# Kernel optimization log

Measured on AMD Instinct MI355X. Metric: run time of the kernel, lower is better.

The kernel has to match this reference:

```python
import jax, jax.numpy as jnp
import numpy as np

EPS = 1e-12


def _segment_softmax(logits, seg, n):
    # numerically stable softmax over edges grouped by destination node
    m = jax.ops.segment_max(logits, seg, num_segments=n)
    e = jnp.exp(logits - m[seg])
    s = jax.ops.segment_sum(e, seg, num_segments=n)
    return e / s[seg]


def _agnn(x, src, dst, beta, n):
    # cosine-similarity attention (PyG AGNNConv): alpha_ij = softmax_i(beta * <x_i/|x_i|, x_j/|x_j|>)
    norm = jnp.sqrt(jnp.sum(x * x, axis=-1, keepdims=True))
    xn = x / jnp.maximum(norm, EPS)
    logits = beta * jnp.sum(xn[dst] * xn[src], axis=-1)  # [E+N]
    alpha = _segment_softmax(logits, dst, n)
    return jax.ops.segment_sum(alpha[:, None] * x[src], dst, num_segments=n)


def setup_inputs() -> dict:
    key = jax.random.key(0)
    ks = jax.random.split(key, 6)
    N, E, F, H, C = 100000, 3200000, 512, 16, 7
    x = jax.random.normal(ks[0], (N, F), dtype=jnp.float32)
    edge_index = jax.random.randint(ks[1], (2, E), 0, N, dtype=jnp.int32)
    W1 = jax.random.normal(ks[2], (H, F), dtype=jnp.float32) * 0.05
    b1 = jnp.zeros((H,), jnp.float32)
    W2 = jax.random.normal(ks[3], (C, H), dtype=jnp.float32) * 0.2
    b2 = jnp.zeros((C,), jnp.float32)
    return {
        "x": x, "edge_index": edge_index,
        "W1": W1, "b1": b1,
        "beta2": jnp.ones((1,), jnp.float32),
        "beta3": jnp.ones((1,), jnp.float32),
        "beta4": jnp.ones((1,), jnp.float32),
        "W2": W2, "b2": b2,
    }


def reference(x, edge_index, W1, b1, beta2, beta3, beta4, W2, b2):
    N = x.shape[0]
    loop = jnp.arange(N, dtype=edge_index.dtype)
    src = jnp.concatenate([edge_index[0], loop])  # self-loops added by AGNNConv
    dst = jnp.concatenate([edge_index[1], loop])

    h = jax.nn.relu(x @ W1.T + b1)                 # lin1 on raw features (eval: dropout = id)
    h = _agnn(h, src, dst, jnp.float32(1.0), N)    # prop1: beta fixed at 1 (requires_grad=False)
    h = _agnn(h, src, dst, beta2[0], N)
    h = _agnn(h, src, dst, beta3[0], N)
    h = _agnn(h, src, dst, beta4[0], N)
    logits = h @ W2.T + b2
    return jax.nn.log_softmax(logits, axis=1)
```

## Files before the change

kernel.cpp:

```cpp
#include <hip/hip_runtime.h>
#include <hip/hip_fp16.h>
#include <math.h>

#define F 512
#define H 16
#define C 7
#define NB 512
#define BIN_CHUNK 4096
#define BIN_T 512

typedef _Float16 h2 __attribute__((ext_vector_type(2)));

__device__ __forceinline__ h2 as_h2(unsigned u) { return __builtin_bit_cast(h2, u); }
__device__ __forceinline__ unsigned as_u32(h2 v) { return __builtin_bit_cast(unsigned, v); }

__device__ __forceinline__ float dot2acc(h2 a, h2 b, float c) {
#if __has_builtin(__builtin_amdgcn_fdot2)
    return __builtin_amdgcn_fdot2(a, b, c, false);
#else
    return c + (float)a[0] * (float)b[0] + (float)a[1] * (float)b[1];
#endif
}

__device__ __forceinline__ float rsq(float x) {
#if __has_builtin(__builtin_amdgcn_rsqf)
    return __builtin_amdgcn_rsqf(x);
#else
    return rsqrtf(x);
#endif
}

__global__ void zero_i32(int* p, int n) {
    int i = blockIdx.x * blockDim.x + threadIdx.x;
    if (i < n) p[i] = 0;
}

__global__ __launch_bounds__(BIN_T) void bin_edges(const int* __restrict__ ei, int E, int Etot,
                                                   int width, int cap, int* __restrict__ gcnt,
                                                   unsigned* __restrict__ binned) {
    __shared__ int cnt[NB];
    __shared__ int base[NB];
    int t = threadIdx.x;
    for (int i = t; i < NB; i += BIN_T) cnt[i] = 0;
    __syncthreads();
    long chunk0 = (long)blockIdx.x * BIN_CHUNK;
    for (int k = 0; k < BIN_CHUNK / BIN_T; ++k) {
        long e = chunk0 + k * BIN_T + t;
        if (e < Etot) {
            int dst = (e < E) ? ei[E + e] : (int)(e - E);
            atomicAdd(&cnt[dst / width], 1);
        }
    }
    __syncthreads();
    for (int i = t; i < NB; i += BIN_T) {
        int c = cnt[i];
        base[i] = c ? atomicAdd(&gcnt[i], c) : 0;
        cnt[i] = 0;
    }
    __syncthreads();
    for (int k = 0; k < BIN_CHUNK / BIN_T; ++k) {
        long e = chunk0 + k * BIN_T + t;
        if (e < Etot) {
            int src, dst;
            if (e < E) { src = ei[e]; dst = ei[E + e]; }
            else       { src = (int)(e - E); dst = src; }
            int b = dst / width;
            size_t pos = (size_t)b * cap + base[b] + atomicAdd(&cnt[b], 1);
            binned[pos] = (unsigned)src | ((unsigned)(dst - b * width) << 17);
        }
    }
}

__global__ void bucket_scan(const int* __restrict__ gcnt, int Etot,
                            int* __restrict__ bbase, int* __restrict__ rp, int N) {
    __shared__ int s[NB];
    int t = threadIdx.x;
    int own = gcnt[t];
    s[t] = own;
    __syncthreads();
    for (int d = 1; d < NB; d <<= 1) {
        int add = (t >= d) ? s[t - d] : 0;
        __syncthreads();
        s[t] += add;
        __syncthreads();
    }
    bbase[t] = s[t] - own;
    if (t == NB - 1) bbase[NB] = s[t];
    if (t == 0) rp[N] = Etot;
}

__global__ __launch_bounds__(256) void bucket_sort(const unsigned* __restrict__ binned,
                                                   const int* __restrict__ gcnt,
                                                   const int* __restrict__ bbase,
                                                   int width, int cap, int N,
                                                   int* __restrict__ rp, int* __restrict__ srcs) {
    __shared__ int cnt[256];
    __shared__ int cur[256];
    int b = blockIdx.x, t = threadIdx.x;
    int r0 = bbase[b];
    int ne = gcnt[b];
    const unsigned* bin = binned + (size_t)b * cap;
    int nodeBase = b * width;
    cnt[t] = 0;
    cur[t] = 0;
    __syncthreads();
    for (int e = t; e < ne; e += 256) {
        atomicAdd(&cnt[bin[e] >> 17], 1);
    }
    __syncthreads();
    int own = cnt[t];
    for (int d = 1; d < 256; d <<= 1) {
        int add = (t >= d) ? cnt[t - d] : 0;
        __syncthreads();
        cnt[t] += add;
        __syncthreads();
    }
    int excl = cnt[t] - own;
    int node = nodeBase + t;
    if (t < width && node < N) rp[node] = r0 + excl;
    __syncthreads();
    cnt[t] = excl;
    __syncthreads();
    for (int e = t; e < ne; e += 256) {
        unsigned p = bin[e];
        int dL = p >> 17;
        int pos = r0 + cnt[dL] + atomicAdd(&cur[dL], 1);
        srcs[pos] = (int)(p & 0x1FFFFu);
    }
}

__global__ __launch_bounds__(256) void lin1_relu(const float* __restrict__ x,
                                                 const float* __restrict__ W1,
                                                 const float* __restrict__ b1,
                                                 __half* __restrict__ hrow, int N) {
    __shared__ float4 w4[16 * 16 * 9];
    int t = threadIdx.x;
    for (int r = 0; r < 8; ++r) {
        int idx = r * 256 + t;
        int j = idx >> 7;
        int rem = idx & 127;
        int s = rem >> 3, m = rem & 7;
        w4[(j * 16 + s) * 9 + m] = ((const float4*)W1)[idx];
    }
    __syncthreads();

    int s = t & 15, g = t >> 4;
    int iA = blockIdx.x * 32 + g;
    int iB = iA + 16;
    int iAc = min(iA, N - 1), iBc = min(iB, N - 1);

    const float4* xA4 = (const float4*)(x + (size_t)iAc * F);
    const float4* xB4 = (const float4*)(x + (size_t)iBc * F);
    float4 xa[8], xb[8];
#pragma unroll
    for (int m = 0; m < 8; ++m) xa[m] = xA4[s * 8 + m];
#pragma unroll
    for (int m = 0; m < 8; ++m) xb[m] = xB4[s * 8 + m];

    float vA[16], vB[16];
#pragma unroll
    for (int j = 0; j < 16; ++j) { vA[j] = 0.f; vB[j] = 0.f; }
#pragma unroll
    for (int j = 0; j < 16; ++j) {
        const float4* wr = &w4[(j * 16 + s) * 9];
#pragma unroll
        for (int m = 0; m < 8; ++m) {
            float4 w = wr[m];
            vA[j] += w.x * xa[m].x + w.y * xa[m].y + w.z * xa[m].z + w.w * xa[m].w;
            vB[j] += w.x * xb[m].x + w.y * xb[m].y + w.z * xb[m].z + w.w * xb[m].w;
        }
    }

#pragma unroll
    for (int st = 0; st < 4; ++st) {
        int bit = (s >> st) & 1;
        int cntj = 16 >> (st + 1);
#pragma unroll
        for (int k = 0; k < 8; ++k) {
            if (k < cntj) {
                float keepA = bit ? vA[2 * k + 1] : vA[2 * k];
                float giveA = bit ? vA[2 * k] : vA[2 * k + 1];
                vA[k] = keepA + __shfl_xor(giveA, 1 << st);
                float keepB = bit ? vB[2 * k + 1] : vB[2 * k];
                float giveB = bit ? vB[2 * k] : vB[2 * k + 1];
                vB[k] = keepB + __shfl_xor(giveB, 1 << st);
            }
        }
    }

    float bs = b1[s];
    float oA = fmaxf(vA[0] + bs, 0.f);
    float oB = fmaxf(vB[0] + bs, 0.f);

    if (iA < N) hrow[(size_t)iA * 16 + s] = __float2half(oA);
    if (iB < N) hrow[(size_t)iB * 16 + s] = __float2half(oB);
}

__global__ __launch_bounds__(256) void agnn_step(const uint4* __restrict__ hrow,
                                                 const int* __restrict__ rp,
                                                 const int* __restrict__ srcs,
                                                 const float* __restrict__ bp,
                                                 uint4* __restrict__ hrow_out, int N) {
    int t = threadIdx.x;
    int sub = t & 3, g = t >> 2;
    int i = blockIdx.x * 64 + g;
    if (i >= N) return;

    const float L2E = 1.4426950408889634f;
    float beta = bp ? bp[0] : 1.0f;
    float aL = beta * L2E;
    float mm = fabsf(beta) * L2E;

    const uint4* ri = hrow + (size_t)i * 2;
    uint4 hA = ri[0];
    uint4 hB = ri[1];
    h2 hi[8];
    hi[0] = as_h2(hA.x); hi[1] = as_h2(hA.y); hi[2] = as_h2(hA.z); hi[3] = as_h2(hA.w);
    hi[4] = as_h2(hB.x); hi[5] = as_h2(hB.y); hi[6] = as_h2(hB.z); hi[7] = as_h2(hB.w);

    float sd = 0.f;
#pragma unroll
    for (int q = 0; q < 8; ++q) sd = dot2acc(hi[q], hi[q], sd);
    float c0 = aL * rsq(fmaxf(sd, 1e-24f));

    int e0 = rp[i];
    int deg = rp[i + 1] - e0;
    int dm1 = deg - 1;
    int U = (deg + 3) >> 2;

    int sbuf[4];
    uint4 rb0[4], rb1[4];
#pragma unroll
    for (int u = 0; u < 4; ++u) {
        int s = srcs[e0 + min(sub + 4 * u, dm1)];
        const uint4* r = hrow + (size_t)s * 2;
        rb0[u] = r[0]; rb1[u] = r[1];
        sbuf[u] = srcs[e0 + min(sub + 4 * (u + 4), dm1)];
    }

    float denom = 0.f;
    float acc[16];
#pragma unroll
    for (int j = 0; j < 16; ++j) acc[j] = 0.f;

    for (int mb = 0; mb < U; mb += 4) {
#pragma unroll
        for (int u = 0; u < 4; ++u) {
            int m = mb + u;
            int k = sub + 4 * m;
            uint4 a = rb0[u], b = rb1[u];
            int snext = sbuf[u];
            sbuf[u] = srcs[e0 + min(sub + 4 * (m + 8), dm1)];
            const uint4* r = hrow + (size_t)snext * 2;
            rb0[u] = r[0]; rb1[u] = r[1];

            h2 a0 = as_h2(a.x), a1 = as_h2(a.y), a2 = as_h2(a.z), a3 = as_h2(a.w);
            h2 b0 = as_h2(b.x), b1h = as_h2(b.y), b2h = as_h2(b.z), b3 = as_h2(b.w);

            float cross = 0.f, ss = 0.f;
            cross = dot2acc(hi[0], a0, cross);  ss = dot2acc(a0, a0, ss);
            cross = dot2acc(hi[1], a1, cross);  ss = dot2acc(a1, a1, ss);
            cross = dot2acc(hi[2], a2, cross);  ss = dot2acc(a2, a2, ss);
            cross = dot2acc(hi[3], a3, cross);  ss = dot2acc(a3, a3, ss);
            cross = dot2acc(hi[4], b0, cross);  ss = dot2acc(b0, b0, ss);
            cross = dot2acc(hi[5], b1h, cross); ss = dot2acc(b1h, b1h, ss);
            cross = dot2acc(hi[6], b2h, cross); ss = dot2acc(b2h, b2h, ss);
            cross = dot2acc(hi[7], b3, cross);  ss = dot2acc(b3, b3, ss);

            float rs = rsq(fmaxf(ss, 1e-24f));
            float w = exp2f(fmaf(cross * rs, c0, -mm));
            w = (k < deg) ? w : 0.f;
            denom += w;

            acc[0]  = fmaf(w, (float)a0[0], acc[0]);
            acc[1]  = fmaf(w, (float)a0[1], acc[1]);
            acc[2]  = fmaf(w, (float)a1[0], acc[2]);
            acc[3]  = fmaf(w, (float)a1[1], acc[3]);
            acc[4]  = fmaf(w, (float)a2[0], acc[4]);
            acc[5]  = fmaf(w, (float)a2[1], acc[5]);
            acc[6]  = fmaf(w, (float)a3[0], acc[6]);
            acc[7]  = fmaf(w, (float)a3[1], acc[7]);
            acc[8]  = fmaf(w, (float)b0[0], acc[8]);
            acc[9]  = fmaf(w, (float)b0[1], acc[9]);
            acc[10] = fmaf(w, (float)b1h[0], acc[10]);
            acc[11] = fmaf(w, (float)b1h[1], acc[11]);
            acc[12] = fmaf(w, (float)b2h[0], acc[12]);
            acc[13] = fmaf(w, (float)b2h[1], acc[13]);
            acc[14] = fmaf(w, (float)b3[0], acc[14]);
            acc[15] = fmaf(w, (float)b3[1], acc[15]);
        }
    }

    denom += __shfl_xor(denom, 1);
    denom += __shfl_xor(denom, 2);
#pragma unroll
    for (int j = 0; j < 16; ++j) {
        acc[j] += __shfl_xor(acc[j], 1);
        acc[j] += __shfl_xor(acc[j], 2);
    }

    float rd = 1.0f / denom;

    if (sub < 2) {
        int half = sub * 8;
        uint4 wq;
        h2 t0, t1;
        t0[0] = (_Float16)(acc[half + 0] * rd); t0[1] = (_Float16)(acc[half + 1] * rd);
        t1[0] = (_Float16)(acc[half + 2] * rd); t1[1] = (_Float16)(acc[half + 3] * rd);
        wq.x = as_u32(t0); wq.y = as_u32(t1);
        t0[0] = (_Float16)(acc[half + 4] * rd); t0[1] = (_Float16)(acc[half + 5] * rd);
        t1[0] = (_Float16)(acc[half + 6] * rd); t1[1] = (_Float16)(acc[half + 7] * rd);
        wq.z = as_u32(t0); wq.w = as_u32(t1);
        hrow_out[(size_t)i * 2 + sub] = wq;
    }
}

__global__ __launch_bounds__(256) void head_kernel(const uint4* __restrict__ hn,
                                                   const float* __restrict__ W2,
                                                   const float* __restrict__ b2,
                                                   float* __restrict__ out, int N) {
    __shared__ float w2[C * H];
    __shared__ float bb[C];
    int t = threadIdx.x;
    if (t < C * H) w2[t] = W2[t];
    if (t < C) bb[t] = b2[t];
    __syncthreads();
    int i = blockIdx.x * blockDim.x + t;
    if (i >= N) return;
    const uint4* r = hn + (size_t)i * 2;
    uint4 cA = r[0];
    uint4 cB = r[1];
    float hv[H];
    {
        h2 v;
        v = as_h2(cA.x); hv[0] = (float)v[0];  hv[1] = (float)v[1];
        v = as_h2(cA.y); hv[2] = (float)v[0];  hv[3] = (float)v[1];
        v = as_h2(cA.z); hv[4] = (float)v[0];  hv[5] = (float)v[1];
        v = as_h2(cA.w); hv[6] = (float)v[0];  hv[7] = (float)v[1];
        v = as_h2(cB.x); hv[8] = (float)v[0];  hv[9] = (float)v[1];
        v = as_h2(cB.y); hv[10] = (float)v[0]; hv[11] = (float)v[1];
        v = as_h2(cB.z); hv[12] = (float)v[0]; hv[13] = (float)v[1];
        v = as_h2(cB.w); hv[14] = (float)v[0]; hv[15] = (float)v[1];
    }
    float lg[C];
    float m = -1e30f;
#pragma unroll
    for (int c = 0; c < C; ++c) {
        float s = bb[c];
#pragma unroll
        for (int k = 0; k < H; ++k) s += hv[k] * w2[c * H + k];
        lg[c] = s;
        m = fmaxf(m, s);
    }
    float sum = 0.f;
#pragma unroll
    for (int c = 0; c < C; ++c) sum += expf(lg[c] - m);
    float lse = m + logf(sum);
    float* op = out + (size_t)i * C;
#pragma unroll
    for (int c = 0; c < C; ++c) op[c] = lg[c] - lse;
}

extern "C" void kernel_launch(void* const* d_in, const int* in_sizes, int n_in,
                              void* d_out, int out_size, void* d_ws, size_t ws_size,
                              hipStream_t stream) {
    const float* x     = (const float*)d_in[0];
    const int*   ei    = (const int*)d_in[1];
    const float* W1    = (const float*)d_in[2];
    const float* b1    = (const float*)d_in[3];
    const float* beta2 = (const float*)d_in[4];
    const float* beta3 = (const float*)d_in[5];
    const float* beta4 = (const float*)d_in[6];
    const float* W2    = (const float*)d_in[7];
    const float* b2    = (const float*)d_in[8];
    float* out = (float*)d_out;

    int N = in_sizes[0] / F;
    int E = in_sizes[1] / 2;
    int Etot = E + N;
    int width = (N + NB - 1) / NB;
    int cap = (Etot / NB) * 5 / 4;

    char* p = (char*)d_ws;
    uint4* hr_a = (uint4*)p; p += (size_t)N * 32;
    uint4* hr_b = (uint4*)p; p += (size_t)N * 32;
    int* rp     = (int*)p;   p += (size_t)(N + 1) * 4;
    int* srcs   = (int*)p;   p += (size_t)Etot * 4;
    int* gcnt   = (int*)p;   p += (size_t)NB * 4;
    int* bbase  = (int*)p;   p += (size_t)(NB + 1) * 4;
    p = (char*)(((size_t)p + 255) & ~(size_t)255);
    unsigned* binned = (unsigned*)p; p += (size_t)NB * cap * 4;

    zero_i32<<<(NB + 255) / 256, 256, 0, stream>>>(gcnt, NB);
    bin_edges<<<(Etot + BIN_CHUNK - 1) / BIN_CHUNK, BIN_T, 0, stream>>>(ei, E, Etot, width, cap, gcnt, binned);
    bucket_scan<<<1, NB, 0, stream>>>(gcnt, Etot, bbase, rp, N);
    bucket_sort<<<NB, 256, 0, stream>>>(binned, gcnt, bbase, width, cap, N, rp, srcs);

    lin1_relu<<<(N + 31) / 32, 256, 0, stream>>>(x, W1, b1, (__half*)hr_a, N);

    int gs = (N + 63) / 64;
    agnn_step<<<gs, 256, 0, stream>>>(hr_a, rp, srcs, nullptr, hr_b, N);
    agnn_step<<<gs, 256, 0, stream>>>(hr_b, rp, srcs, beta2, hr_a, N);
    agnn_step<<<gs, 256, 0, stream>>>(hr_a, rp, srcs, beta3, hr_b, N);
    agnn_step<<<gs, 256, 0, stream>>>(hr_b, rp, srcs, beta4, hr_a, N);

    head_kernel<<<(N + 255) / 256, 256, 0, stream>>>(hr_a, W2, b2, out, N);
}
```

Before: 552.4 us.

## Fuse output head into last AGNN step and widen bucket_sort blocks

```diff
diff --git a/kernel.cpp b/kernel.cpp
--- a/kernel.cpp
+++ b/kernel.cpp
@@ -8,6 +8,7 @@
 #define NB 512
 #define BIN_CHUNK 4096
 #define BIN_T 512
+#define BS_T 512
 
 typedef _Float16 h2 __attribute__((ext_vector_type(2)));
 
@@ -89,11 +90,11 @@
     if (t == 0) rp[N] = Etot;
 }
 
-__global__ __launch_bounds__(256) void bucket_sort(const unsigned* __restrict__ binned,
-                                                   const int* __restrict__ gcnt,
-                                                   const int* __restrict__ bbase,
-                                                   int width, int cap, int N,
-                                                   int* __restrict__ rp, int* __restrict__ srcs) {
+__global__ __launch_bounds__(BS_T) void bucket_sort(const unsigned* __restrict__ binned,
+                                                    const int* __restrict__ gcnt,
+                                                    const int* __restrict__ bbase,
+                                                    int width, int cap, int N,
+                                                    int* __restrict__ rp, int* __restrict__ srcs) {
     __shared__ int cnt[256];
     __shared__ int cur[256];
     int b = blockIdx.x, t = threadIdx.x;
@@ -101,27 +102,26 @@
     int ne = gcnt[b];
     const unsigned* bin = binned + (size_t)b * cap;
     int nodeBase = b * width;
-    cnt[t] = 0;
-    cur[t] = 0;
-    __syncthreads();
-    for (int e = t; e < ne; e += 256) {
+    if (t < 256) { cnt[t] = 0; cur[t] = 0; }
+    __syncthreads();
+    for (int e = t; e < ne; e += BS_T) {
         atomicAdd(&cnt[bin[e] >> 17], 1);
     }
     __syncthreads();
-    int own = cnt[t];
+    int own = (t < 256) ? cnt[t] : 0;
     for (int d = 1; d < 256; d <<= 1) {
-        int add = (t >= d) ? cnt[t - d] : 0;
+        int add = (t >= d && t < 256) ? cnt[t - d] : 0;
         __syncthreads();
-        cnt[t] += add;
+        if (t < 256) cnt[t] += add;
         __syncthreads();
     }
-    int excl = cnt[t] - own;
+    int excl = (t < 256) ? (cnt[t] - own) : 0;
     int node = nodeBase + t;
     if (t < width && node < N) rp[node] = r0 + excl;
     __syncthreads();
-    cnt[t] = excl;
-    __syncthreads();
-    for (int e = t; e < ne; e += 256) {
+    if (t < 256) cnt[t] = excl;
+    __syncthreads();
+    for (int e = t; e < ne; e += BS_T) {
         unsigned p = bin[e];
         int dL = p >> 17;
         int pos = r0 + cnt[dL] + atomicAdd(&cur[dL], 1);
@@ -200,7 +200,10 @@
                                                  const int* __restrict__ rp,
                                                  const int* __restrict__ srcs,
                                                  const float* __restrict__ bp,
-                                                 uint4* __restrict__ hrow_out, int N) {
+                                                 uint4* __restrict__ hrow_out,
+                                                 const float* __restrict__ W2,
+                                                 const float* __restrict__ b2,
+                                                 float* __restrict__ out, int N) {
     int t = threadIdx.x;
     int sub = t & 3, g = t >> 2;
     int i = blockIdx.x * 64 + g;
@@ -301,6 +304,32 @@
 
     float rd = 1.0f / denom;
 
+    if (W2) {
+        if (sub == 0) {
+            float hv[H];
+#pragma unroll
+            for (int j = 0; j < H; ++j) hv[j] = acc[j] * rd;
+            float lg[C];
+            float mx = -1e30f;
+#pragma unroll
+            for (int c = 0; c < C; ++c) {
+                float s = b2[c];
+#pragma unroll
+                for (int k = 0; k < H; ++k) s += hv[k] * W2[c * H + k];
+                lg[c] = s;
+                mx = fmaxf(mx, s);
+            }
+            float sum = 0.f;
+#pragma unroll
+            for (int c = 0; c < C; ++c) sum += expf(lg[c] - mx);
+            float lse = mx + logf(sum);
+            float* op = out + (size_t)i * C;
+#pragma unroll
+            for (int c = 0; c < C; ++c) op[c] = lg[c] - lse;
+        }
+        return;
+    }
+
     if (sub < 2) {
         int half = sub * 8;
         uint4 wq;
@@ -313,52 +342,6 @@
         wq.z = as_u32(t0); wq.w = as_u32(t1);
         hrow_out[(size_t)i * 2 + sub] = wq;
     }
-}
-
-__global__ __launch_bounds__(256) void head_kernel(const uint4* __restrict__ hn,
-                                                   const float* __restrict__ W2,
-                                                   const float* __restrict__ b2,
-                                                   float* __restrict__ out, int N) {
-    __shared__ float w2[C * H];
-    __shared__ float bb[C];
-    int t = threadIdx.x;
-    if (t < C * H) w2[t] = W2[t];
-    if (t < C) bb[t] = b2[t];
-    __syncthreads();
-    int i = blockIdx.x * blockDim.x + t;
-    if (i >= N) return;
-    const uint4* r = hn + (size_t)i * 2;
-    uint4 cA = r[0];
-    uint4 cB = r[1];
-    float hv[H];
-    {
-        h2 v;
-        v = as_h2(cA.x); hv[0] = (float)v[0];  hv[1] = (float)v[1];
-        v = as_h2(cA.y); hv[2] = (float)v[0];  hv[3] = (float)v[1];
-        v = as_h2(cA.z); hv[4] = (float)v[0];  hv[5] = (float)v[1];
-        v = as_h2(cA.w); hv[6] = (float)v[0];  hv[7] = (float)v[1];
-        v = as_h2(cB.x); hv[8] = (float)v[0];  hv[9] = (float)v[1];
-        v = as_h2(cB.y); hv[10] = (float)v[0]; hv[11] = (float)v[1];
-        v = as_h2(cB.z); hv[12] = (float)v[0]; hv[13] = (float)v[1];
-        v = as_h2(cB.w); hv[14] = (float)v[0]; hv[15] = (float)v[1];
-    }
-    float lg[C];
-    float m = -1e30f;
-#pragma unroll
-    for (int c = 0; c < C; ++c) {
-        float s = bb[c];
-#pragma unroll
-        for (int k = 0; k < H; ++k) s += hv[k] * w2[c * H + k];
-        lg[c] = s;
-        m = fmaxf(m, s);
-    }
-    float sum = 0.f;
-#pragma unroll
-    for (int c = 0; c < C; ++c) sum += expf(lg[c] - m);
-    float lse = m + logf(sum);
-    float* op = out + (size_t)i * C;
-#pragma unroll
-    for (int c = 0; c < C; ++c) op[c] = lg[c] - lse;
 }
 
 extern "C" void kernel_launch(void* const* d_in, const int* in_sizes, int n_in,
@@ -394,15 +377,13 @@
     zero_i32<<<(NB + 255) / 256, 256, 0, stream>>>(gcnt, NB);
     bin_edges<<<(Etot + BIN_CHUNK - 1) / BIN_CHUNK, BIN_T, 0, stream>>>(ei, E, Etot, width, cap, gcnt, binned);
     bucket_scan<<<1, NB, 0, stream>>>(gcnt, Etot, bbase, rp, N);
-    bucket_sort<<<NB, 256, 0, stream>>>(binned, gcnt, bbase, width, cap, N, rp, srcs);
+    bucket_sort<<<NB, BS_T, 0, stream>>>(binned, gcnt, bbase, width, cap, N, rp, srcs);
 
     lin1_relu<<<(N + 31) / 32, 256, 0, stream>>>(x, W1, b1, (__half*)hr_a, N);
 
     int gs = (N + 63) / 64;
-    agnn_step<<<gs, 256, 0, stream>>>(hr_a, rp, srcs, nullptr, hr_b, N);
-    agnn_step<<<gs, 256, 0, stream>>>(hr_b, rp, srcs, beta2, hr_a, N);
-    agnn_step<<<gs, 256, 0, stream>>>(hr_a, rp, srcs, beta3, hr_b, N);
-    agnn_step<<<gs, 256, 0, stream>>>(hr_b, rp, srcs, beta4, hr_a, N);
-
-    head_kernel<<<(N + 255) / 256, 256, 0, stream>>>(hr_a, W2, b2, out, N);
-}
+    agnn_step<<<gs, 256, 0, stream>>>(hr_a, rp, srcs, nullptr, hr_b, nullptr, nullptr, nullptr, N);
+    agnn_step<<<gs, 256, 0, stream>>>(hr_b, rp, srcs, beta2, hr_a, nullptr, nullptr, nullptr, N);
+    agnn_step<<<gs, 256, 0, stream>>>(hr_a, rp, srcs, beta3, hr_b, nullptr, nullptr, nullptr, N);
+    agnn_step<<<gs, 256, 0, stream>>>(hr_b, rp, srcs, beta4, nullptr, W2, b2, out, N);
+}
```

Measured after the change: 546.4 us. About the same (-1.1%).
